# Kernel optimization log

Hardware: AMD Instinct MI355X
Metric: run time of the kernel (lower is better)

Reference implementation:

```python
import jax, jax.numpy as jnp
import numpy as np

NUM_NODES = 100000
NUM_EDGES = 400000
F_IN = 16          # num_node_features
F_EDGE = 8         # num_edge_features
EMB = 16           # emb_size
NUM_GRAPHS = 256


def setup_inputs() -> dict:
    key = jax.random.key(0)
    ks = jax.random.split(key, 12)
    x = jax.random.normal(ks[0], (NUM_NODES, F_IN), dtype=jnp.float32)
    edge_index = jax.random.randint(ks[1], (2, NUM_EDGES), 0, NUM_NODES, dtype=jnp.int32)
    edge_attr = jax.random.normal(ks[2], (NUM_EDGES, F_EDGE), dtype=jnp.float32)
    batch = jnp.sort(jax.random.randint(ks[3], (NUM_NODES,), 0, NUM_GRAPHS, dtype=jnp.int32))
    s = 0.1
    # edge-network MLP: Linear(F_EDGE -> F_IN*EMB) + ReLU (torch Linear convention: W[out,in])
    nn1_w = jax.random.normal(ks[4], (F_IN * EMB, F_EDGE), dtype=jnp.float32) * s
    nn1_b = jax.random.normal(ks[5], (F_IN * EMB,), dtype=jnp.float32) * s
    # NNConv root weight (bias=False Linear) + separate bias
    root_w = jax.random.normal(ks[6], (EMB, F_IN), dtype=jnp.float32) * s
    conv_b = jax.random.normal(ks[7], (EMB,), dtype=jnp.float32) * s
    lin1_w = jax.random.normal(ks[8], (EMB, 2 * EMB), dtype=jnp.float32) * s
    lin1_b = jax.random.normal(ks[9], (EMB,), dtype=jnp.float32) * s
    lin2_w = jax.random.normal(ks[10], (1, EMB), dtype=jnp.float32) * s
    lin2_b = jax.random.normal(ks[11], (1,), dtype=jnp.float32) * s
    return {"x": x, "edge_index": edge_index, "edge_attr": edge_attr, "batch": batch,
            "nn1_w": nn1_w, "nn1_b": nn1_b, "root_w": root_w, "conv_b": conv_b,
            "lin1_w": lin1_w, "lin1_b": lin1_b, "lin2_w": lin2_w, "lin2_b": lin2_b}


def reference(x, edge_index, edge_attr, batch, nn1_w, nn1_b, root_w, conv_b,
              lin1_w, lin1_b, lin2_w, lin2_b):
    N = x.shape[0]
    src, dst = edge_index[0], edge_index[1]  # PyG: message flows src(j) -> dst(i)
    # edge network -> per-edge weight matrices [E, F_IN, EMB]
    w = jax.nn.relu(edge_attr @ nn1_w.T + nn1_b).reshape(-1, F_IN, EMB)
    # gather source features, per-edge matmul
    msg = jnp.einsum('ei,eio->eo', x[src], w)  # [E, EMB]
    # scatter-mean into target nodes
    sums = jax.ops.segment_sum(msg, dst, num_segments=N)
    cnt = jax.ops.segment_sum(jnp.ones((msg.shape[0],), msg.dtype), dst, num_segments=N)
    agg = sums / jnp.maximum(cnt, 1.0)[:, None]
    # NNConv: root transform + aggregated messages + bias, then outer ReLU
    h = jax.nn.relu(agg + x @ root_w.T + conv_b)  # [N, EMB]
    # global max pool and global mean pool per graph
    gmax = jax.ops.segment_max(h, batch, num_segments=NUM_GRAPHS)
    gsum = jax.ops.segment_sum(h, batch, num_segments=NUM_GRAPHS)
    gcnt = jax.ops.segment_sum(jnp.ones((N,), h.dtype), batch, num_segments=NUM_GRAPHS)
    gmean = gsum / jnp.maximum(gcnt, 1.0)[:, None]
    pooled = jnp.concatenate([gmax, gmean], axis=1)  # [G, 2*EMB]
    h2 = jax.nn.relu(pooled @ lin1_w.T + lin1_b)
    out = h2 @ lin2_w.T + lin2_b  # [G, 1]
    return out
```

## Files before the change

### kernel.cpp

```cpp
#include <hip/hip_runtime.h>

#define NUM_NODES 100000
#define NUM_EDGES 400000
#define F_IN 16
#define F_EDGE 8
#define EMB 16
#define NUM_GRAPHS 256

#define EDGE_TILES 5
#define EDGE_BLOCKS (NUM_EDGES / (32 * EDGE_TILES))

#define NPB 128
#define NODE_BLOCKS ((NUM_NODES + NPB - 1) / NPB)


__global__ __launch_bounds__(256) void edge_kernel(
    const float* __restrict__ x, const int* __restrict__ ei,
    const float* __restrict__ ea, const float* __restrict__ nn1_w,
    const float* __restrict__ nn1_b, float* __restrict__ sums,
    float* __restrict__ cnt)
{
    __shared__ float wtp[256 * 12];
    __shared__ float btp[16 * 20];

    const int tid = threadIdx.x;
    const int eL  = tid >> 4;
    const int o   = tid & 15;

    #pragma unroll
    for (int t = tid; t < F_IN * EMB * F_EDGE; t += 256)
        wtp[(t >> 3) * 12 + (t & 7)] = nn1_w[t];
    btp[(tid & 15) * 20 + (tid >> 4)] = nn1_b[tid];
    __syncthreads();

    float br[F_IN];
    #pragma unroll
    for (int r = 0; r < 4; r++) {
        const float4 b4 = *(const float4*)&btp[o * 20 + 4 * r];
        br[4 * r + 0] = b4.x; br[4 * r + 1] = b4.y;
        br[4 * r + 2] = b4.z; br[4 * r + 3] = b4.w;
    }

    for (int t = 0; t < EDGE_TILES; t++) {
        const int e0 = (blockIdx.x * EDGE_TILES + t) * 32;
        const int eA = e0 + eL;
        const int eB = e0 + 16 + eL;

        const int srcA = ei[eA];
        const int srcB = ei[eB];
        const int dstA = ei[NUM_EDGES + eA];
        const int dstB = ei[NUM_EDGES + eB];

        const float4 a00 = *(const float4*)&ea[eA * 8];
        const float4 a01 = *(const float4*)&ea[eA * 8 + 4];
        const float4 a10 = *(const float4*)&ea[eB * 8];
        const float4 a11 = *(const float4*)&ea[eB * 8 + 4];

        float xr0[F_IN], xr1[F_IN];
        #pragma unroll
        for (int r = 0; r < 4; r++) {
            const float4 v0 = *(const float4*)&x[srcA * 16 + 4 * r];
            const float4 v1 = *(const float4*)&x[srcB * 16 + 4 * r];
            xr0[4 * r + 0] = v0.x; xr0[4 * r + 1] = v0.y;
            xr0[4 * r + 2] = v0.z; xr0[4 * r + 3] = v0.w;
            xr1[4 * r + 0] = v1.x; xr1[4 * r + 1] = v1.y;
            xr1[4 * r + 2] = v1.z; xr1[4 * r + 3] = v1.w;
        }

        float acc0 = 0.f, acc1 = 0.f;
        #pragma unroll
        for (int i = 0; i < F_IN; i++) {
            const float* wr = &wtp[(i * 16 + o) * 12];
            const float4 w0 = *(const float4*)wr;
            const float4 w1 = *(const float4*)(wr + 4);
            float u = br[i];
            u = fmaf(a00.x, w0.x, u); u = fmaf(a00.y, w0.y, u);
            u = fmaf(a00.z, w0.z, u); u = fmaf(a00.w, w0.w, u);
            u = fmaf(a01.x, w1.x, u); u = fmaf(a01.y, w1.y, u);
            u = fmaf(a01.z, w1.z, u); u = fmaf(a01.w, w1.w, u);
            acc0 = fmaf(xr0[i], fmaxf(u, 0.f), acc0);
            float v = br[i];
            v = fmaf(a10.x, w0.x, v); v = fmaf(a10.y, w0.y, v);
            v = fmaf(a10.z, w0.z, v); v = fmaf(a10.w, w0.w, v);
            v = fmaf(a11.x, w1.x, v); v = fmaf(a11.y, w1.y, v);
            v = fmaf(a11.z, w1.z, v); v = fmaf(a11.w, w1.w, v);
            acc1 = fmaf(xr1[i], fmaxf(v, 0.f), acc1);
        }

        atomicAdd(&sums[dstA * 16 + o], acc0);
        atomicAdd(&sums[dstB * 16 + o], acc1);
        if (o == 0) {
            atomicAdd(&cnt[dstA], 1.f);
            atomicAdd(&cnt[dstB], 1.f);
        }
    }
}

__global__ __launch_bounds__(256) void node_kernel(
    const float* __restrict__ x, const int* __restrict__ batch,
    const float* __restrict__ root_w, const float* __restrict__ conv_b,
    const float* __restrict__ sums, const float* __restrict__ cnt,
    unsigned int* __restrict__ gmax, float* __restrict__ gsum,
    float* __restrict__ gcnt)
{
    __shared__ float rwT[256];
    __shared__ float xsh[256];
    __shared__ float ssh[256];
    __shared__ float csh[16];
    __shared__ int   bsh[16];
    __shared__ float hsh[256];

    const int tid = threadIdx.x;
    const int j   = tid >> 4;
    const int o   = tid & 15;
    const int n0  = blockIdx.x * NPB;

    rwT[(tid & 15) * 16 + (tid >> 4)] = root_w[tid];
    const float cb = conv_b[o];

    int   curg = batch[n0];
    float am = 0.f, asum = 0.f, ac = 0.f;

    for (int s0 = 0; s0 < NPB; s0 += 16) {
        const int base = n0 + s0;
        const int idx  = base * 16 + tid;
        const bool v   = (idx < NUM_NODES * 16);
        const float xv = v ? x[idx]    : 0.f;
        const float sv = v ? sums[idx] : 0.f;
        float cv = 1.f; int bv = -1;
        if (tid < 16) {
            const int n = base + tid;
            if (n < NUM_NODES) { cv = cnt[n]; bv = batch[n]; }
        }
        __syncthreads();
        xsh[tid] = xv; ssh[tid] = sv;
        if (tid < 16) { csh[tid] = cv; bsh[tid] = bv; }
        __syncthreads();

        float a = cb + ssh[j * 16 + o] / fmaxf(csh[j], 1.f);
        #pragma unroll
        for (int i = 0; i < F_IN; i++)
            a = fmaf(xsh[j * 16 + i], rwT[i * 16 + o], a);
        hsh[tid] = fmaxf(a, 0.f);
        __syncthreads();

        if (tid < 16) {
            #pragma unroll 1
            for (int jj = 0; jj < 16; jj++) {
                const int g = bsh[jj];
                if (g < 0) break;
                if (g != curg) {
                    atomicMax(&gmax[curg * 16 + o], __float_as_uint(am));
                    atomicAdd(&gsum[curg * 16 + o], asum);
                    if (o == 0) atomicAdd(&gcnt[curg], ac);
                    am = 0.f; asum = 0.f; ac = 0.f; curg = g;
                }
                const float h = hsh[jj * 16 + o];
                am = fmaxf(am, h); asum += h; ac += 1.f;
            }
        }
    }

    if (tid < 16) {
        atomicMax(&gmax[curg * 16 + o], __float_as_uint(am));
        atomicAdd(&gsum[curg * 16 + o], asum);
        if (o == 0) atomicAdd(&gcnt[curg], ac);
    }
}

__global__ __launch_bounds__(256) void head_kernel(
    const unsigned int* __restrict__ gmax, const float* __restrict__ gsum,
    const float* __restrict__ gcnt,
    const float* __restrict__ lin1_w, const float* __restrict__ lin1_b,
    const float* __restrict__ lin2_w, const float* __restrict__ lin2_b,
    float* __restrict__ out)
{
    const int g = threadIdx.x;

    float pooled[2 * EMB];
    #pragma unroll
    for (int o = 0; o < EMB; o++) pooled[o] = __uint_as_float(gmax[g * 16 + o]);
    const float c = fmaxf(gcnt[g], 1.f);
    #pragma unroll
    for (int o = 0; o < EMB; o++) pooled[EMB + o] = gsum[g * 16 + o] / c;

    float acc = lin2_b[0];
    #pragma unroll
    for (int k = 0; k < EMB; k++) {
        float a = lin1_b[k];
        #pragma unroll
        for (int cc = 0; cc < 2 * EMB; cc++)
            a = fmaf(pooled[cc], lin1_w[k * 32 + cc], a);
        acc = fmaf(fmaxf(a, 0.f), lin2_w[k], acc);
    }
    out[g] = acc;
}

extern "C" void kernel_launch(void* const* d_in, const int* in_sizes, int n_in,
                              void* d_out, int out_size, void* d_ws, size_t ws_size,
                              hipStream_t stream) {
    const float* x      = (const float*)d_in[0];
    const int*   ei     = (const int*)d_in[1];
    const float* ea     = (const float*)d_in[2];
    const int*   batch  = (const int*)d_in[3];
    const float* nn1_w  = (const float*)d_in[4];
    const float* nn1_b  = (const float*)d_in[5];
    const float* root_w = (const float*)d_in[6];
    const float* conv_b = (const float*)d_in[7];
    const float* lin1_w = (const float*)d_in[8];
    const float* lin1_b = (const float*)d_in[9];
    const float* lin2_w = (const float*)d_in[10];
    const float* lin2_b = (const float*)d_in[11];
    float* out = (float*)d_out;

    float*        sums = (float*)d_ws;
    float*        cnt  = sums + (size_t)NUM_NODES * EMB;
    unsigned int* gmax = (unsigned int*)(cnt + NUM_NODES);
    float*        gsum = (float*)(gmax + NUM_GRAPHS * EMB);
    float*        gcnt = gsum + NUM_GRAPHS * EMB;

    const size_t zero_bytes = sizeof(float) *
        ((size_t)NUM_NODES * EMB + NUM_NODES + 2 * NUM_GRAPHS * EMB + NUM_GRAPHS);
    hipMemsetAsync(d_ws, 0, zero_bytes, stream);

    edge_kernel<<<EDGE_BLOCKS, 256, 0, stream>>>(x, ei, ea, nn1_w, nn1_b, sums, cnt);
    node_kernel<<<NODE_BLOCKS, 256, 0, stream>>>(
        x, batch, root_w, conv_b, sums, cnt, gmax, gsum, gcnt);
    head_kernel<<<1, 256, 0, stream>>>(gmax, gsum, gcnt,
                                       lin1_w, lin1_b, lin2_w, lin2_b, out);
}
```

Baseline: 164.7 us.

## Double-buffer edge tile loads and prefetch source indices in edge kernel

Result: no change. 165.9 us (+0.7%).

```diff
diff --git a/kernel.cpp b/kernel.cpp
--- a/kernel.cpp
+++ b/kernel.cpp
@@ -14,7 +14,7 @@
 #define NODE_BLOCKS ((NUM_NODES + NPB - 1) / NPB)
 
 
-__global__ __launch_bounds__(256) void edge_kernel(
+__global__ __launch_bounds__(256, 3) void edge_kernel(
     const float* __restrict__ x, const int* __restrict__ ei,
     const float* __restrict__ ea, const float* __restrict__ nn1_w,
     const float* __restrict__ nn1_b, float* __restrict__ sums,
@@ -26,10 +26,21 @@
     const int tid = threadIdx.x;
     const int eL  = tid >> 4;
     const int o   = tid & 15;
-
-    #pragma unroll
-    for (int t = tid; t < F_IN * EMB * F_EDGE; t += 256)
-        wtp[(t >> 3) * 12 + (t & 7)] = nn1_w[t];
+    const int eb0 = blockIdx.x * EDGE_TILES * 32;
+
+    int srcA[EDGE_TILES], srcB[EDGE_TILES];
+    #pragma unroll
+    for (int t = 0; t < EDGE_TILES; t++) {
+        srcA[t] = ei[eb0 + t * 32 + eL];
+        srcB[t] = ei[eb0 + t * 32 + 16 + eL];
+    }
+
+    {
+        const float4 w0 = *(const float4*)&nn1_w[tid * 8];
+        const float4 w1 = *(const float4*)&nn1_w[tid * 8 + 4];
+        *(float4*)&wtp[tid * 12]     = w0;
+        *(float4*)&wtp[tid * 12 + 4] = w1;
+    }
     btp[(tid & 15) * 20 + (tid >> 4)] = nn1_b[tid];
     __syncthreads();
 
@@ -41,59 +52,72 @@
         br[4 * r + 2] = b4.z; br[4 * r + 3] = b4.w;
     }
 
+    float4 pA00, pA01, pA10, pA11; float pX0[16], pX1[16]; int pDA, pDB;
+    float4 qA00, qA01, qA10, qA11; float qX0[16], qX1[16]; int qDA, qDB;
+
+#define LOAD_TILE(T, A00, A01, A10, A11, X0, X1, DA, DB) do {               \
+        const int eA_ = eb0 + (T) * 32 + eL;                                \
+        const int eB_ = eA_ + 16;                                           \
+        DA = ei[NUM_EDGES + eA_];                                           \
+        DB = ei[NUM_EDGES + eB_];                                           \
+        A00 = *(const float4*)&ea[eA_ * 8];                                 \
+        A01 = *(const float4*)&ea[eA_ * 8 + 4];                             \
+        A10 = *(const float4*)&ea[eB_ * 8];                                 \
+        A11 = *(const float4*)&ea[eB_ * 8 + 4];                             \
+        _Pragma("unroll")                                                   \
+        for (int r = 0; r < 4; r++) {                                       \
+            const float4 v0 = *(const float4*)&x[srcA[T] * 16 + 4 * r];     \
+            const float4 v1 = *(const float4*)&x[srcB[T] * 16 + 4 * r];     \
+            X0[4*r+0] = v0.x; X0[4*r+1] = v0.y;                             \
+            X0[4*r+2] = v0.z; X0[4*r+3] = v0.w;                             \
+            X1[4*r+0] = v1.x; X1[4*r+1] = v1.y;                             \
+            X1[4*r+2] = v1.z; X1[4*r+3] = v1.w;                             \
+        }                                                                   \
+    } while (0)
+
+#define COMPUTE_TILE(A00, A01, A10, A11, X0, X1, DA, DB) do {               \
+        float acc0 = 0.f, acc1 = 0.f;                                       \
+        _Pragma("unroll")                                                   \
+        for (int i = 0; i < F_IN; i++) {                                    \
+            const float* wr = &wtp[(i * 16 + o) * 12];                      \
+            const float4 w0 = *(const float4*)wr;                           \
+            const float4 w1 = *(const float4*)(wr + 4);                     \
+            float u = br[i];                                                \
+            u = fmaf(A00.x, w0.x, u); u = fmaf(A00.y, w0.y, u);             \
+            u = fmaf(A00.z, w0.z, u); u = fmaf(A00.w, w0.w, u);             \
+            u = fmaf(A01.x, w1.x, u); u = fmaf(A01.y, w1.y, u);             \
+            u = fmaf(A01.z, w1.z, u); u = fmaf(A01.w, w1.w, u);             \
+            acc0 = fmaf(X0[i], fmaxf(u, 0.f), acc0);                        \
+            float v = br[i];                                                \
+            v = fmaf(A10.x, w0.x, v); v = fmaf(A10.y, w0.y, v);             \
+            v = fmaf(A10.z, w0.z, v); v = fmaf(A10.w, w0.w, v);             \
+            v = fmaf(A11.x, w1.x, v); v = fmaf(A11.y, w1.y, v);             \
+            v = fmaf(A11.z, w1.z, v); v = fmaf(A11.w, w1.w, v);             \
+            acc1 = fmaf(X1[i], fmaxf(v, 0.f), acc1);                        \
+        }                                                                   \
+        atomicAdd(&sums[DA * 16 + o], acc0);                                \
+        atomicAdd(&sums[DB * 16 + o], acc1);                                \
+        if (o == 0) {                                                       \
+            atomicAdd(&cnt[DA], 1.f);                                       \
+            atomicAdd(&cnt[DB], 1.f);                                       \
+        }                                                                   \
+    } while (0)
+
+    LOAD_TILE(0, pA00, pA01, pA10, pA11, pX0, pX1, pDA, pDB);
+    #pragma unroll
     for (int t = 0; t < EDGE_TILES; t++) {
-        const int e0 = (blockIdx.x * EDGE_TILES + t) * 32;
-        const int eA = e0 + eL;
-        const int eB = e0 + 16 + eL;
-
-        const int srcA = ei[eA];
-        const int srcB = ei[eB];
-        const int dstA = ei[NUM_EDGES + eA];
-        const int dstB = ei[NUM_EDGES + eB];
-
-        const float4 a00 = *(const float4*)&ea[eA * 8];
-        const float4 a01 = *(const float4*)&ea[eA * 8 + 4];
-        const float4 a10 = *(const float4*)&ea[eB * 8];
-        const float4 a11 = *(const float4*)&ea[eB * 8 + 4];
-
-        float xr0[F_IN], xr1[F_IN];
-        #pragma unroll
-        for (int r = 0; r < 4; r++) {
-            const float4 v0 = *(const float4*)&x[srcA * 16 + 4 * r];
-            const float4 v1 = *(const float4*)&x[srcB * 16 + 4 * r];
-            xr0[4 * r + 0] = v0.x; xr0[4 * r + 1] = v0.y;
-            xr0[4 * r + 2] = v0.z; xr0[4 * r + 3] = v0.w;
-            xr1[4 * r + 0] = v1.x; xr1[4 * r + 1] = v1.y;
-            xr1[4 * r + 2] = v1.z; xr1[4 * r + 3] = v1.w;
+        if ((t & 1) == 0) {
+            if (t + 1 < EDGE_TILES)
+                LOAD_TILE(t + 1, qA00, qA01, qA10, qA11, qX0, qX1, qDA, qDB);
+            COMPUTE_TILE(pA00, pA01, pA10, pA11, pX0, pX1, pDA, pDB);
+        } else {
+            if (t + 1 < EDGE_TILES)
+                LOAD_TILE(t + 1, pA00, pA01, pA10, pA11, pX0, pX1, pDA, pDB);
+            COMPUTE_TILE(qA00, qA01, qA10, qA11, qX0, qX1, qDA, qDB);
         }
-
-        float acc0 = 0.f, acc1 = 0.f;
-        #pragma unroll
-        for (int i = 0; i < F_IN; i++) {
-            const float* wr = &wtp[(i * 16 + o) * 12];
-            const float4 w0 = *(const float4*)wr;
-            const float4 w1 = *(const float4*)(wr + 4);
-            float u = br[i];
-            u = fmaf(a00.x, w0.x, u); u = fmaf(a00.y, w0.y, u);
-            u = fmaf(a00.z, w0.z, u); u = fmaf(a00.w, w0.w, u);
-            u = fmaf(a01.x, w1.x, u); u = fmaf(a01.y, w1.y, u);
-            u = fmaf(a01.z, w1.z, u); u = fmaf(a01.w, w1.w, u);
-            acc0 = fmaf(xr0[i], fmaxf(u, 0.f), acc0);
-            float v = br[i];
-            v = fmaf(a10.x, w0.x, v); v = fmaf(a10.y, w0.y, v);
-            v = fmaf(a10.z, w0.z, v); v = fmaf(a10.w, w0.w, v);
-            v = fmaf(a11.x, w1.x, v); v = fmaf(a11.y, w1.y, v);
-            v = fmaf(a11.z, w1.z, v); v = fmaf(a11.w, w1.w, v);
-            acc1 = fmaf(xr1[i], fmaxf(v, 0.f), acc1);
-        }
-
-        atomicAdd(&sums[dstA * 16 + o], acc0);
-        atomicAdd(&sums[dstB * 16 + o], acc1);
-        if (o == 0) {
-            atomicAdd(&cnt[dstA], 1.f);
-            atomicAdd(&cnt[dstB], 1.f);
-        }
-    }
+    }
+#undef LOAD_TILE
+#undef COMPUTE_TILE
 }
 
 __global__ __launch_bounds__(256) void node_kernel(
```
